# Optimization experiments

Measured on AMD Instinct MI355X. Metric: run time of the kernel, lower is better.

## Reference

```python
import jax, jax.numpy as jnp
import numpy as np

B, S, D, M, E, K = 2, 2048, 1024, 1408, 8, 2  # batch, seq, n_embed, n_moe_mlp, n_experts, top_k


def setup_inputs() -> dict:
    key = jax.random.key(0)
    k0, k1, k2, k3, k4 = jax.random.split(key, 5)
    scale = 0.02
    return {
        "x": jax.random.normal(k0, (B, S, D), dtype=jnp.float32),
        "w_gate": jax.random.normal(k1, (D, E), dtype=jnp.float32) * scale,  # gate.weight.T
        "w_g": jax.random.normal(k2, (E, D, M), dtype=jnp.float32) * scale,  # gate_proj.weight.T per expert
        "w_u": jax.random.normal(k3, (E, D, M), dtype=jnp.float32) * scale,  # up_proj.weight.T per expert
        "w_d": jax.random.normal(k4, (E, M, D), dtype=jnp.float32) * scale,  # down_proj.weight.T per expert
    }


def reference(x, w_gate, w_g, w_u, w_d):
    # router
    scores = x @ w_gate                                  # [B,S,E]
    topk_scores, topk_idx = jax.lax.top_k(scores, K)     # [B,S,K]
    topk_probs = jax.nn.softmax(topk_scores, axis=-1)    # softmax over selected experts only
    # scatter top-k probs back to dense [B,S,E] gating (top_k indices are distinct)
    gating = jnp.sum(
        jax.nn.one_hot(topk_idx, E, dtype=topk_probs.dtype) * topk_probs[..., None],
        axis=-2,
    )                                                    # [B,S,E]
    # dense all-expert SwiGLU (faithful to the compute-then-mask original)
    hidden = jax.nn.silu(jnp.einsum("bsd,edm->ebsm", x, w_g)) * jnp.einsum(
        "bsd,edm->ebsm", x, w_u
    )                                                    # [E,B,S,M]
    expert_out = jnp.einsum("ebsm,emd->ebsd", hidden, w_d)  # [E,B,S,D]
    # masked weighted combine
    y = jnp.einsum("bse,ebsd->bsd", gating, expert_out)  # [B,S,D]
    return y
```

## Files before the change

kernel.cpp:

```cpp
#include <hip/hip_runtime.h>
#include <cstdio>

constexpr int T  = 4096;
constexpr int D  = 1024;
constexpr int M  = 1408;
constexpr int E  = 8;

constexpr int TM = 128;
constexpr int TN = 128;
constexpr int BK = 32;
constexpr int RCAP = T * 2 + E * TM;
constexpr int MT_MAX = T / TM;
constexpr int NT_UP = M / TN;
constexpr int NT_DN = D / TN;

constexpr int CSTR = 64;
constexpr int TOKB = 16;
constexpr int RTB  = T / TOKB;
constexpr int XCV  = (T * D) / 2048;
constexpr int TP_PER_W = (M / 32) * (D / 32) * E;
constexpr int PREP_GRID = RTB + XCV + 3 * TP_PER_W;

typedef _Float16 half8 __attribute__((ext_vector_type(8)));
typedef _Float16 half4 __attribute__((ext_vector_type(4)));
typedef float    floatx4 __attribute__((ext_vector_type(4)));

constexpr size_t OFF_COUNTS = 0;
constexpr size_t OFF_BASE   = (size_t)E * CSTR * 4;
constexpr size_t OFF_PC     = OFF_BASE + 64;
constexpr size_t OFF_TOTAL  = OFF_PC + 64;
constexpr size_t OFF_T2E    = OFF_TOTAL + 64;
constexpr size_t OFF_T2POS  = OFF_T2E   + (size_t)2 * T * 4;
constexpr size_t OFF_T2P    = OFF_T2POS + (size_t)2 * T * 4;
constexpr size_t OFF_TLIST  = OFF_T2P   + (size_t)2 * T * 4;
constexpr size_t OFF_XG     = OFF_TLIST + (size_t)E * T * 4;
constexpr size_t OFF_HID    = OFF_XG  + (size_t)RCAP * D * 2;
constexpr size_t OFF_WGT    = OFF_HID + (size_t)RCAP * M * 2;
constexpr size_t OFF_WUT    = OFF_WGT + (size_t)E * M * D * 2;
constexpr size_t OFF_WDT    = OFF_WUT + (size_t)E * M * D * 2;
constexpr size_t WS_NEED    = OFF_WDT + (size_t)E * D * M * 2;

__device__ __forceinline__ void gl_lds16(const void* g, void* l) {
  __builtin_amdgcn_global_load_lds(
      (const __attribute__((address_space(1))) unsigned int*)g,
      (__attribute__((address_space(3))) unsigned int*)l, 16, 0, 0);
}

__device__ __forceinline__ void expert_base_pc(const int* __restrict__ counts,
                                               int e, int& base_e, int& pc_e,
                                               int& cnt_e) {
  int b = 0; base_e = 0; pc_e = 0; cnt_e = 0;
  #pragma unroll
  for (int ee = 0; ee < E; ++ee) {
    int c = counts[ee * CSTR];
    int p = (c + TM - 1) / TM * TM;
    if (ee == e) { base_e = b; pc_e = p; cnt_e = c; }
    b += p;
  }
}

__global__ __launch_bounds__(256) void k_prep(
    const float* __restrict__ x, const float* __restrict__ wgate,
    const float* __restrict__ w_g, const float* __restrict__ w_u,
    const float* __restrict__ w_d,
    _Float16* __restrict__ Xh,
    _Float16* __restrict__ wgT, _Float16* __restrict__ wuT, _Float16* __restrict__ wdT,
    int* __restrict__ counts, int* __restrict__ tlist,
    int* __restrict__ t2e, int* __restrict__ t2pos, float* __restrict__ t2p) {
  __shared__ float tile[32][33];
  __shared__ int   s_cnt[E];
  __shared__ int   s_base[E];
  __shared__ int   s_e[2 * TOKB];
  __shared__ int   s_pos[2 * TOKB];
  __shared__ float s_p[2 * TOKB];
  int bid = blockIdx.x;

  if (bid < RTB) {
    int wv = threadIdx.x >> 6, lane = threadIdx.x & 63;
    if (threadIdx.x < E) s_cnt[threadIdx.x] = 0;
    __syncthreads();
    for (int j = 0; j < TOKB / 4; ++j) {
      int tl = wv * (TOKB / 4) + j;
      int t  = bid * TOKB + tl;
      const float* xr = x + (size_t)t * D;
      float acc[E] = {0.f,0.f,0.f,0.f,0.f,0.f,0.f,0.f};
      #pragma unroll
      for (int i = 0; i < D / 64; ++i) {
        int d = i * 64 + lane;
        float xv = xr[d];
        const float4* wr2 = (const float4*)(wgate + (size_t)d * E);
        float4 w0 = wr2[0], w1 = wr2[1];
        acc[0] += xv * w0.x; acc[1] += xv * w0.y; acc[2] += xv * w0.z; acc[3] += xv * w0.w;
        acc[4] += xv * w1.x; acc[5] += xv * w1.y; acc[6] += xv * w1.z; acc[7] += xv * w1.w;
      }
      #pragma unroll
      for (int e = 0; e < E; ++e) {
        #pragma unroll
        for (int off = 32; off; off >>= 1) acc[e] += __shfl_xor(acc[e], off, 64);
      }
      if (lane == 0) {
        int i0 = 0; float s0 = acc[0];
        #pragma unroll
        for (int e = 1; e < E; ++e) if (acc[e] > s0) { s0 = acc[e]; i0 = e; }
        int i1 = -1; float s1 = -1e30f;
        #pragma unroll
        for (int e = 0; e < E; ++e) if (e != i0 && acc[e] > s1) { s1 = acc[e]; i1 = e; }
        float p0 = 1.f / (1.f + expf(s1 - s0));
        float p1 = 1.f - p0;
        int q0 = atomicAdd(&s_cnt[i0], 1);
        int q1 = atomicAdd(&s_cnt[i1], 1);
        s_e[2 * tl]     = i0; s_pos[2 * tl]     = q0; s_p[2 * tl]     = p0;
        s_e[2 * tl + 1] = i1; s_pos[2 * tl + 1] = q1; s_p[2 * tl + 1] = p1;
      }
    }
    __syncthreads();
    if (threadIdx.x < E)
      s_base[threadIdx.x] = atomicAdd(&counts[threadIdx.x * CSTR], s_cnt[threadIdx.x]);
    __syncthreads();
    if (threadIdx.x < 2 * TOKB) {
      int sl = threadIdx.x;
      int e = s_e[sl];
      int pos = s_base[e] + s_pos[sl];
      int t = bid * TOKB + (sl >> 1);
      tlist[e * T + pos] = t;
      t2e[2 * t + (sl & 1)]   = e;
      t2pos[2 * t + (sl & 1)] = pos;
      t2p[2 * t + (sl & 1)]   = s_p[sl];
    }
    return;
  }

  if (bid < RTB + XCV) {
    size_t base = (size_t)(bid - RTB) * 2048 + threadIdx.x * 8;
    float4 v0 = *(const float4*)(x + base);
    float4 v1 = *(const float4*)(x + base + 4);
    half8 h;
    h[0] = (_Float16)v0.x; h[1] = (_Float16)v0.y;
    h[2] = (_Float16)v0.z; h[3] = (_Float16)v0.w;
    h[4] = (_Float16)v1.x; h[5] = (_Float16)v1.y;
    h[6] = (_Float16)v1.z; h[7] = (_Float16)v1.w;
    *(half8*)(Xh + base) = h;
    return;
  }

  int i = bid - RTB - XCV;
  int which = i / TP_PER_W;
  int j = i - which * TP_PER_W;
  const float* src; _Float16* dst; int Rr, Cc;
  if (which == 0)      { src = w_g; dst = wgT; Rr = D; Cc = M; }
  else if (which == 1) { src = w_u; dst = wuT; Rr = D; Cc = M; }
  else                 { src = w_d; dst = wdT; Rr = M; Cc = D; }
  int ctn = Cc / 32, rtn = Rr / 32;
  int e   = j / (ctn * rtn);
  int rem = j - e * (ctn * rtn);
  int rt = rem / ctn, ct = rem - rt * ctn;
  int tr  = threadIdx.x >> 3;
  int tc4 = (threadIdx.x & 7) * 4;
  const float* s = src + ((size_t)e * Rr + rt * 32 + tr) * Cc + ct * 32 + tc4;
  float4 v = *(const float4*)s;
  tile[tr][tc4 + 0] = v.x; tile[tr][tc4 + 1] = v.y;
  tile[tr][tc4 + 2] = v.z; tile[tr][tc4 + 3] = v.w;
  __syncthreads();
  union { _Float16 h[4]; ushort4 u; } o;
  #pragma unroll
  for (int q = 0; q < 4; ++q) o.h[q] = (_Float16)tile[tc4 + q][tr];
  *(ushort4*)(dst + ((size_t)e * Cc + ct * 32 + tr) * Rr + rt * 32 + tc4) = o.u;
}

__global__ __launch_bounds__(256, 2) void k_upgate(
    const _Float16* __restrict__ Xh, const _Float16* __restrict__ wgT,
    const _Float16* __restrict__ wuT, _Float16* __restrict__ Hid,
    const int* __restrict__ counts, const int* __restrict__ tlist) {
  int lin = blockIdx.x;
  int e = lin & 7;
  int r = lin >> 3;
  int nt = r % NT_UP;
  int mt = r / NT_UP;
  int base_e, pc_e, cnt_e;
  expert_base_pc(counts, e, base_e, pc_e, cnt_e);
  if (mt * TM >= pc_e) return;
  int row0 = base_e + mt * TM;
  int n0 = nt * TN;
  __shared__ _Float16 As[2][TM * BK];
  __shared__ _Float16 Bg[2][TN * BK];
  __shared__ _Float16 Bu[2][TN * BK];
  int tid = threadIdx.x;
  int w = tid >> 6, lane = tid & 63;
  int lrow = lane & 15, quad = lane >> 4;
  int wr = w >> 1, wc = w & 1;
  int sr = lane >> 2;
  int c4 = lane & 3;
  int swc = ((c4 ^ ((sr >> 1) & 3))) * 8;

  const _Float16* wg_e = wgT + (size_t)e * M * D;
  const _Float16* wu_e = wuT + (size_t)e * M * D;
  const _Float16* pA[2]; const _Float16* pG[2]; const _Float16* pU[2];
  int loff[2];
  #pragma unroll
  for (int is = 0; is < 2; ++is) {
    int grow = w * 32 + is * 16 + sr;
    int local = mt * TM + grow;
    int trow = (local < cnt_e) ? tlist[e * T + local] : 0;
    pA[is] = Xh   + (size_t)trow * D + swc;
    pG[is] = wg_e + (size_t)(n0 + grow) * D + swc;
    pU[is] = wu_e + (size_t)(n0 + grow) * D + swc;
    loff[is] = (w * 2 + is) * 1024;
  }

  int swr = (lrow >> 1) & 3;

  floatx4 accg[4][4] = {};
  floatx4 accu[4][4] = {};

  auto stage = [&](int b) {
    char* a0 = (char*)&As[b][0];
    char* g0 = (char*)&Bg[b][0];
    char* u0 = (char*)&Bu[b][0];
    #pragma unroll
    for (int is = 0; is < 2; ++is) {
      gl_lds16(pA[is], a0 + loff[is]); pA[is] += BK;
      gl_lds16(pG[is], g0 + loff[is]); pG[is] += BK;
      gl_lds16(pU[is], u0 + loff[is]); pU[is] += BK;
    }
  };
  auto compute = [&](int b) {
    int kc = (quad ^ swr) * 8;
    half8 af[4];
    #pragma unroll
    for (int i = 0; i < 4; ++i)
      af[i] = *(const half8*)&As[b][(wr * 64 + i * 16 + lrow) * BK + kc];
    #pragma unroll
    for (int c = 0; c < 4; ++c) {
      int bo = (wc * 64 + c * 16 + lrow) * BK + kc;
      half8 bgc = *(const half8*)&Bg[b][bo];
      half8 buc = *(const half8*)&Bu[b][bo];
      #pragma unroll
      for (int i = 0; i < 4; ++i) {
        accg[c][i] = __builtin_amdgcn_mfma_f32_16x16x32_f16(af[i], bgc, accg[c][i], 0, 0, 0);
        accu[c][i] = __builtin_amdgcn_mfma_f32_16x16x32_f16(af[i], buc, accu[c][i], 0, 0, 0);
      }
    }
  };

  stage(0);
  __syncthreads();
  int cur = 0;
  for (int kt = 1; kt < D / BK; ++kt) {
    stage(cur ^ 1);
    compute(cur);
    __syncthreads();
    cur ^= 1;
  }
  compute(cur);

  #pragma unroll
  for (int c = 0; c < 4; ++c) {
    int col = n0 + wc * 64 + c * 16 + lrow;
    #pragma unroll
    for (int i = 0; i < 4; ++i) {
      int rowb = row0 + wr * 64 + i * 16 + quad * 4;
      #pragma unroll
      for (int reg = 0; reg < 4; ++reg) {
        float g = accg[c][i][reg], u = accu[c][i][reg];
        Hid[(size_t)(rowb + reg) * M + col] = (_Float16)(g / (1.f + expf(-g)) * u);
      }
    }
  }
}

__global__ __launch_bounds__(256, 2) void k_down(
    const _Float16* __restrict__ Hid, const _Float16* __restrict__ wdT,
    _Float16* __restrict__ Yp, const int* __restrict__ counts) {
  int lin = blockIdx.x;
  int e = lin & 7;
  int r = lin >> 3;
  int nt = r % NT_DN;
  int mt = r / NT_DN;
  int base_e, pc_e, cnt_e;
  expert_base_pc(counts, e, base_e, pc_e, cnt_e);
  if (mt * TM >= pc_e) return;
  int row0 = base_e + mt * TM;
  int d0 = nt * TN;
  __shared__ _Float16 As[2][TM * BK];
  __shared__ _Float16 Bs[2][TN * BK];
  int tid = threadIdx.x;
  int w = tid >> 6, lane = tid & 63;
  int lrow = lane & 15, quad = lane >> 4;
  int wr = w >> 1, wc = w & 1;
  int sr = lane >> 2;
  int c4 = lane & 3;
  int swc = ((c4 ^ ((sr >> 1) & 3))) * 8;

  const _Float16* wd_e = wdT + (size_t)e * D * M;
  const _Float16* pA[2]; const _Float16* pB[2];
  int loff[2];
  #pragma unroll
  for (int is = 0; is < 2; ++is) {
    int grow = w * 32 + is * 16 + sr;
    pA[is] = Hid  + (size_t)(row0 + grow) * M + swc;
    pB[is] = wd_e + (size_t)(d0   + grow) * M + swc;
    loff[is] = (w * 2 + is) * 1024;
  }

  int swr = (lrow >> 1) & 3;

  floatx4 acc[4][4] = {};

  auto stage = [&](int b) {
    char* a0 = (char*)&As[b][0];
    char* b0 = (char*)&Bs[b][0];
    #pragma unroll
    for (int is = 0; is < 2; ++is) {
      gl_lds16(pA[is], a0 + loff[is]); pA[is] += BK;
      gl_lds16(pB[is], b0 + loff[is]); pB[is] += BK;
    }
  };
  auto compute = [&](int b) {
    int kc = (quad ^ swr) * 8;
    half8 af[4];
    #pragma unroll
    for (int i = 0; i < 4; ++i)
      af[i] = *(const half8*)&As[b][(wr * 64 + i * 16 + lrow) * BK + kc];
    #pragma unroll
    for (int c = 0; c < 4; ++c) {
      half8 bc = *(const half8*)&Bs[b][(wc * 64 + c * 16 + lrow) * BK + kc];
      #pragma unroll
      for (int i = 0; i < 4; ++i)
        acc[c][i] = __builtin_amdgcn_mfma_f32_16x16x32_f16(af[i], bc, acc[c][i], 0, 0, 0);
    }
  };

  stage(0);
  __syncthreads();
  int cur = 0;
  for (int kt = 1; kt < M / BK; ++kt) {
    stage(cur ^ 1);
    compute(cur);
    __syncthreads();
    cur ^= 1;
  }
  compute(cur);

  #pragma unroll
  for (int c = 0; c < 4; ++c) {
    int col = d0 + wc * 64 + c * 16 + lrow;
    #pragma unroll
    for (int i = 0; i < 4; ++i) {
      int rowb = row0 + wr * 64 + i * 16 + quad * 4;
      #pragma unroll
      for (int reg = 0; reg < 4; ++reg)
        Yp[(size_t)(rowb + reg) * D + col] = (_Float16)acc[c][i][reg];
    }
  }
}

__global__ __launch_bounds__(256) void k_combine(
    const _Float16* __restrict__ Yp, const int* __restrict__ counts,
    const int* __restrict__ t2e, const int* __restrict__ t2pos,
    const float* __restrict__ t2p, float* __restrict__ out) {
  int t = blockIdx.x;
  int e0 = t2e[2 * t], e1 = t2e[2 * t + 1];
  int b = 0, b0 = 0, b1 = 0;
  #pragma unroll
  for (int ee = 0; ee < E; ++ee) {
    if (ee == e0) b0 = b;
    if (ee == e1) b1 = b;
    int c = counts[ee * CSTR];
    b += (c + TM - 1) / TM * TM;
  }
  int r0 = b0 + t2pos[2 * t];
  int r1 = b1 + t2pos[2 * t + 1];
  float p0 = t2p[2 * t], p1 = t2p[2 * t + 1];
  int d = threadIdx.x * 4;
  half4 h0 = *(const half4*)(Yp + (size_t)r0 * D + d);
  half4 h1 = *(const half4*)(Yp + (size_t)r1 * D + d);
  float4 o;
  o.x = p0 * (float)h0.x + p1 * (float)h1.x;
  o.y = p0 * (float)h0.y + p1 * (float)h1.y;
  o.z = p0 * (float)h0.z + p1 * (float)h1.z;
  o.w = p0 * (float)h0.w + p1 * (float)h1.w;
  *(float4*)(out + (size_t)t * D + d) = o;
}

extern "C" void kernel_launch(void* const* d_in, const int* in_sizes, int n_in,
                              void* d_out, int out_size, void* d_ws, size_t ws_size,
                              hipStream_t stream) {
  const float* x     = (const float*)d_in[0];
  const float* wgate = (const float*)d_in[1];
  const float* w_g   = (const float*)d_in[2];
  const float* w_u   = (const float*)d_in[3];
  const float* w_d   = (const float*)d_in[4];
  float* out = (float*)d_out;
  char* ws = (char*)d_ws;

  if (ws_size < WS_NEED) {
    fprintf(stderr, "kernel_launch: ws_size=%zu < needed %zu\n", ws_size, WS_NEED);
    return;
  }

  int* counts = (int*)(ws + OFF_COUNTS);
  int* t2e    = (int*)(ws + OFF_T2E);
  int* t2pos  = (int*)(ws + OFF_T2POS);
  float* t2p  = (float*)(ws + OFF_T2P);
  int* tlist  = (int*)(ws + OFF_TLIST);
  _Float16* Xh  = (_Float16*)(ws + OFF_XG);
  _Float16* Hid = (_Float16*)(ws + OFF_HID);
  _Float16* wgT = (_Float16*)(ws + OFF_WGT);
  _Float16* wuT = (_Float16*)(ws + OFF_WUT);
  _Float16* wdT = (_Float16*)(ws + OFF_WDT);

  hipMemsetAsync(counts, 0, (size_t)E * CSTR * 4, stream);

  k_prep<<<PREP_GRID, 256, 0, stream>>>(x, wgate, w_g, w_u, w_d, Xh,
                                        wgT, wuT, wdT,
                                        counts, tlist, t2e, t2pos, t2p);
  k_upgate<<<E * MT_MAX * NT_UP, 256, 0, stream>>>(Xh, wgT, wuT, Hid, counts, tlist);
  _Float16* Yp = Xh;
  k_down<<<E * MT_MAX * NT_DN, 256, 0, stream>>>(Hid, wdT, Yp, counts);
  k_combine<<<T, 256, 0, stream>>>(Yp, counts, t2e, t2pos, t2p, out);
}
```

Before: 308.9 us.

## Use triple-buffered LDS pipeline with explicit vmcnt waits in expert GEMMs

The up/gate and down GEMM kernels move from double-buffered LDS with full __syncthreads to a three-stage ring. Loads run two tiles ahead, and explicit s_waitcnt vmcnt waits let later tiles' global-to-LDS loads stay in flight during compute. The weight-transpose prep blocks also each handle four 32x32 tiles instead of one, which cuts the block count. The cost is 50% more LDS per block, which may lower occupancy, and hand-tuned wait counts that must match the number of loads issued per stage.

```diff
diff --git a/kernel.cpp b/kernel.cpp
--- a/kernel.cpp
+++ b/kernel.cpp
@@ -18,12 +18,18 @@
 constexpr int TOKB = 16;
 constexpr int RTB  = T / TOKB;
 constexpr int XCV  = (T * D) / 2048;
-constexpr int TP_PER_W = (M / 32) * (D / 32) * E;
+constexpr int TP_PER_W = E * 2816 / 8;
 constexpr int PREP_GRID = RTB + XCV + 3 * TP_PER_W;
 
 typedef _Float16 half8 __attribute__((ext_vector_type(8)));
 typedef _Float16 half4 __attribute__((ext_vector_type(4)));
 typedef float    floatx4 __attribute__((ext_vector_type(4)));
+
+#define VMW12() asm volatile("s_waitcnt vmcnt(12)" ::: "memory")
+#define VMW8()  asm volatile("s_waitcnt vmcnt(8)"  ::: "memory")
+#define VMW6()  asm volatile("s_waitcnt vmcnt(6)"  ::: "memory")
+#define VMW4()  asm volatile("s_waitcnt vmcnt(4)"  ::: "memory")
+#define VMW0()  asm volatile("s_waitcnt vmcnt(0)"  ::: "memory")
 
 constexpr size_t OFF_COUNTS = 0;
 constexpr size_t OFF_BASE   = (size_t)E * CSTR * 4;
@@ -67,7 +73,7 @@
     _Float16* __restrict__ wgT, _Float16* __restrict__ wuT, _Float16* __restrict__ wdT,
     int* __restrict__ counts, int* __restrict__ tlist,
     int* __restrict__ t2e, int* __restrict__ t2pos, float* __restrict__ t2p) {
-  __shared__ float tile[32][33];
+  __shared__ float tile[4][32][33];
   __shared__ int   s_cnt[E];
   __shared__ int   s_base[E];
   __shared__ int   s_e[2 * TOKB];
@@ -150,21 +156,29 @@
   if (which == 0)      { src = w_g; dst = wgT; Rr = D; Cc = M; }
   else if (which == 1) { src = w_u; dst = wuT; Rr = D; Cc = M; }
   else                 { src = w_d; dst = wdT; Rr = M; Cc = D; }
-  int ctn = Cc / 32, rtn = Rr / 32;
+  int ctn = Cc / 128, rtn = Rr / 32;
   int e   = j / (ctn * rtn);
   int rem = j - e * (ctn * rtn);
   int rt = rem / ctn, ct = rem - rt * ctn;
   int tr  = threadIdx.x >> 3;
   int tc4 = (threadIdx.x & 7) * 4;
-  const float* s = src + ((size_t)e * Rr + rt * 32 + tr) * Cc + ct * 32 + tc4;
-  float4 v = *(const float4*)s;
-  tile[tr][tc4 + 0] = v.x; tile[tr][tc4 + 1] = v.y;
-  tile[tr][tc4 + 2] = v.z; tile[tr][tc4 + 3] = v.w;
+  const float* s = src + ((size_t)e * Rr + rt * 32 + tr) * Cc + ct * 128 + tc4;
+  float4 v[4];
+  #pragma unroll
+  for (int q = 0; q < 4; ++q) v[q] = *(const float4*)(s + q * 32);
+  #pragma unroll
+  for (int q = 0; q < 4; ++q) {
+    tile[q][tr][tc4 + 0] = v[q].x; tile[q][tr][tc4 + 1] = v[q].y;
+    tile[q][tr][tc4 + 2] = v[q].z; tile[q][tr][tc4 + 3] = v[q].w;
+  }
   __syncthreads();
-  union { _Float16 h[4]; ushort4 u; } o;
-  #pragma unroll
-  for (int q = 0; q < 4; ++q) o.h[q] = (_Float16)tile[tc4 + q][tr];
-  *(ushort4*)(dst + ((size_t)e * Cc + ct * 32 + tr) * Rr + rt * 32 + tc4) = o.u;
+  #pragma unroll
+  for (int q = 0; q < 4; ++q) {
+    union { _Float16 h[4]; ushort4 u; } o;
+    #pragma unroll
+    for (int p = 0; p < 4; ++p) o.h[p] = (_Float16)tile[q][tc4 + p][tr];
+    *(ushort4*)(dst + ((size_t)e * Cc + ct * 128 + q * 32 + tr) * Rr + rt * 32 + tc4) = o.u;
+  }
 }
 
 __global__ __launch_bounds__(256, 2) void k_upgate(
@@ -181,9 +195,9 @@
   if (mt * TM >= pc_e) return;
   int row0 = base_e + mt * TM;
   int n0 = nt * TN;
-  __shared__ _Float16 As[2][TM * BK];
-  __shared__ _Float16 Bg[2][TN * BK];
-  __shared__ _Float16 Bu[2][TN * BK];
+  __shared__ _Float16 As[3][TM * BK];
+  __shared__ _Float16 Bg[3][TN * BK];
+  __shared__ _Float16 Bu[3][TN * BK];
   int tid = threadIdx.x;
   int w = tid >> 6, lane = tid & 63;
   int lrow = lane & 15, quad = lane >> 4;
@@ -242,16 +256,22 @@
     }
   };
 
-  stage(0);
-  __syncthreads();
-  int cur = 0;
-  for (int kt = 1; kt < D / BK; ++kt) {
-    stage(cur ^ 1);
-    compute(cur);
-    __syncthreads();
-    cur ^= 1;
-  }
-  compute(cur);
+  constexpr int NTK = D / BK;
+  stage(0); stage(1);
+  for (int k = 0; k < NTK; ++k) {
+    if (k + 2 < NTK) {
+      stage((k + 2) % 3);
+      VMW12();
+    } else if (k + 1 < NTK) {
+      VMW6();
+    } else {
+      VMW0();
+    }
+    __builtin_amdgcn_sched_barrier(0);
+    __builtin_amdgcn_s_barrier();
+    compute(k % 3);
+    __builtin_amdgcn_s_barrier();
+  }
 
   #pragma unroll
   for (int c = 0; c < 4; ++c) {
@@ -281,8 +301,8 @@
   if (mt * TM >= pc_e) return;
   int row0 = base_e + mt * TM;
   int d0 = nt * TN;
-  __shared__ _Float16 As[2][TM * BK];
-  __shared__ _Float16 Bs[2][TN * BK];
+  __shared__ _Float16 As[3][TM * BK];
+  __shared__ _Float16 Bs[3][TN * BK];
   int tid = threadIdx.x;
   int w = tid >> 6, lane = tid & 63;
   int lrow = lane & 15, quad = lane >> 4;
@@ -330,16 +350,22 @@
     }
   };
 
-  stage(0);
-  __syncthreads();
-  int cur = 0;
-  for (int kt = 1; kt < M / BK; ++kt) {
-    stage(cur ^ 1);
-    compute(cur);
-    __syncthreads();
-    cur ^= 1;
-  }
-  compute(cur);
+  constexpr int NTK = M / BK;
+  stage(0); stage(1);
+  for (int k = 0; k < NTK; ++k) {
+    if (k + 2 < NTK) {
+      stage((k + 2) % 3);
+      VMW8();
+    } else if (k + 1 < NTK) {
+      VMW4();
+    } else {
+      VMW0();
+    }
+    __builtin_amdgcn_sched_barrier(0);
+    __builtin_amdgcn_s_barrier();
+    compute(k % 3);
+    __builtin_amdgcn_s_barrier();
+  }
 
   #pragma unroll
   for (int c = 0; c < 4; ++c) {
```

After: 297.8 us. 1.04x faster.
